# Kernel tuning notes

Hardware: AMD Instinct MI355X
Metric: run time of the kernel (lower is better)

Reference implementation:

```python
import jax, jax.numpy as jnp
import numpy as np

# PEPS hyper-parameters (match init_kwargs)
L1 = 6
L2 = 6
D_PHYS = 2   # d: physical dimension
D_BOND = 6   # D: virtual bond dimension
DC = 24      # Dc: boundary-MPS truncation cutoff
BATCH = 32


def setup_inputs() -> dict:
    key = jax.random.key(0)
    k1, k2 = jax.random.split(key)
    tensors = jax.random.normal(
        k1, (L1, L2, D_PHYS, D_BOND, D_BOND, D_BOND, D_BOND), dtype=jnp.float32)
    configs = jax.random.randint(k2, (BATCH, L1 * L2), 0, D_PHYS, dtype=jnp.int32)
    return {"configs": configs, "tensors": tensors}


def _site(tensors, configs, l1, l2):
    # Gather per-sample site tensor: [b, left, up, down, right]
    t = tensors[l1, l2][configs[:, l1 * L2 + l2].astype(jnp.int32)]
    if l2 == 0:
        t = t[:, :1]
    if l1 == 0:
        t = t[:, :, :1]
    if l1 == L1 - 1:
        t = t[:, :, :, :1]
    if l2 == L2 - 1:
        t = t[:, :, :, :, :1]
    return t


def _qr(a):
    # Reduced QR that also supports wide matrices (m < n) in a way that has
    # a JAX-differentiable definition: Q comes from the QR of the first m
    # columns (identical to Householder QR of the full matrix), and
    # R[:, m:] = Q^T A[:, m:].
    m, n = a.shape[-2], a.shape[-1]
    if m >= n:
        return jnp.linalg.qr(a)
    q, r1 = jnp.linalg.qr(a[..., :m])
    r2 = jnp.matmul(jnp.swapaxes(q, -1, -2), a[..., m:])
    return q, jnp.concatenate([r1, r2], axis=-1)


def _bmps(line1, line2):
    # Contract row of boundary MPS with next PEPS row: [b,l,L,u,d,r,R]
    double = [jnp.einsum('blumr,bLmdR->blLudrR', t1, t2)
              for t1, t2 in zip(line1, line2)]
    b = double[0].shape[0]
    s0 = double[0].shape
    double[0] = double[0].reshape(b, s0[1] * s0[2], s0[3], s0[4], s0[5], s0[6])
    # Left-to-right QR canonicalization sweep
    for j in range(L2 - 1):
        t = double[j]
        _, l, u, dn, r, R = t.shape
        q, rmat = _qr(t.reshape(b, l * u * dn, r * R))
        k = q.shape[-1]
        double[j] = q.reshape(b, l, u, dn, k)
        remain = rmat.reshape(b, k, r, R)
        double[j + 1] = jnp.einsum('bkmM,bmMudrR->bkudrR', remain, double[j + 1])
    tlast = double[-1]
    sl = tlast.shape
    double[-1] = tlast.reshape(b, sl[1], sl[2], sl[3], sl[4] * sl[5])
    # Right-to-left truncated-SVD compression sweep
    for j in range(L2 - 1, 0, -1):
        t = double[j]
        _, l, u, dn, r = t.shape
        U, S, Vh = jnp.linalg.svd(t.reshape(b, l, u * dn * r), full_matrices=False)
        if S.shape[-1] > DC:
            U = U[:, :, :DC]
            S = S[:, :DC]
            Vh = Vh[:, :DC, :]
        double[j] = Vh.reshape(b, -1, u, dn, r)
        double[j - 1] = jnp.einsum('bludm,bmr,br->bludr', double[j - 1], U, S)
    return double


def _forward(configs, tensors):
    rows = [[_site(tensors, configs, i, j) for j in range(L2)] for i in range(L1)]
    cand = rows[0]
    for i in range(1, L1):
        cand = _bmps(cand, rows[i])
    res = cand[0]
    for j in range(1, L2):
        res = res * cand[j]  # all [b,1,1,1,1] after the final row
    return res[:, 0, 0, 0, 0]


def reference(configs, tensors):
    return _forward(configs, tensors)
```

## Files before the change

### kernel.cpp

```cpp
#include <hip/hip_runtime.h>
#include <math.h>

#define NT 1024
#define NB 32

#define M_D    0
#define M_A    124416
#define M_A3   248832
#define M_Q2   373248
#define M_Q4   404352
#define M_TB   435456
#define M_Q1   456192
#define M_Q0   457488
#define M_ROW  457552
#define M_R    463168
#define M_T    483904
#define M_T3   504640
#define M_G    525392
#define M_CA   546128
#define M_CB   554840
#define M_X    563552
#define M_Z    567008
#define M_T5   570464
#define M_X5   570680
#define M_QP   570896
#define M_X1   570960
#define M_T1   571024
#define M_Y0   571888
#define M_YH   575344
#define M_W    578800
#define M_P    579376
#define M_STRIDE 582832

__device__ __align__(16) double g_m[(size_t)NB * M_STRIDE];

#define STAGE_CAP 82944
#define LO_J     82944
#define LO_NORM  88128
#define LO_S     89280
#define LO_E     89472
#define LO_E2    90624
#define LO_SEL   91776
#define LO_FLAG  91872
#define LO_LOG   91880
#define LO_SCALE 91888
#define LDS_BYTES 92160

__device__ __forceinline__ char* ldsp() {
  extern __shared__ char lds_pool[];
  return lds_pool;
}
#define L_B(p)     ((float*)(p))
#define L_J(p)     ((float*)((p)+LO_J))
#define L_ZR(p)    ((double*)(p))
#define L_J24(p)   ((double*)((p)+28800))
#define L_NORM(p)  ((double*)((p)+LO_NORM))
#define L_S(p)     ((double*)((p)+LO_S))
#define L_E(p)     ((double*)((p)+LO_E))
#define L_E2(p)    ((double*)((p)+LO_E2))
#define L_SEL(p)   ((int*)((p)+LO_SEL))
#define L_FLAG(p)  ((int*)((p)+LO_FLAG))
#define L_LOG(p)   ((double*)((p)+LO_LOG))
#define L_SCALE(p) ((double*)((p)+LO_SCALE))

__device__ void mm_nn(const double* __restrict__ A, int lda, const double* __restrict__ Bm, int ldb,
                      double* __restrict__ C, int ldc, int M, int N, int Kd, int tid) {
  if ((N & 3) == 0) {
    int nstrip = N >> 2;
    for (int u = tid; u < M * nstrip; u += NT) {
      int i = u / nstrip, j0 = (u - i * nstrip) << 2;
      const double* a = A + (size_t)i * lda;
      const double* b = Bm + j0;
      double d0 = 0, d1 = 0, d2 = 0, d3 = 0;
      for (int k = 0; k < Kd; ++k) {
        double av = a[k];
        const double* br = b + (size_t)k * ldb;
        d0 += av * br[0]; d1 += av * br[1]; d2 += av * br[2]; d3 += av * br[3];
      }
      size_t o = (size_t)i * ldc + j0;
      C[o] = d0; C[o + 1] = d1; C[o + 2] = d2; C[o + 3] = d3;
    }
  } else {
    for (int idx = tid; idx < M * N; idx += NT) {
      int i = idx / N, j = idx - i * N;
      const double* a = A + (size_t)i * lda;
      double acc = 0.0;
      for (int k = 0; k < Kd; ++k) acc += a[k] * Bm[(size_t)k * ldb + j];
      C[(size_t)i * ldc + j] = acc;
    }
  }
  __syncthreads();
}

__device__ void mm_tn(const double* __restrict__ A, int lda, const double* __restrict__ Bm, int ldb,
                      double* __restrict__ C, int ldc, int M, int N, int Kd, int tid) {
  if ((N & 3) == 0) {
    int nstrip = N >> 2;
    for (int u = tid; u < M * nstrip; u += NT) {
      int i = u / nstrip, j0 = (u - i * nstrip) << 2;
      double d0 = 0, d1 = 0, d2 = 0, d3 = 0;
      for (int k = 0; k < Kd; ++k) {
        double av = A[(size_t)k * lda + i];
        const double* br = Bm + (size_t)k * ldb + j0;
        d0 += av * br[0]; d1 += av * br[1]; d2 += av * br[2]; d3 += av * br[3];
      }
      size_t o = (size_t)i * ldc + j0;
      C[o] = d0; C[o + 1] = d1; C[o + 2] = d2; C[o + 3] = d3;
    }
  } else {
    for (int idx = tid; idx < M * N; idx += NT) {
      int i = idx / N, j = idx - i * N;
      double acc = 0.0;
      for (int k = 0; k < Kd; ++k) acc += A[(size_t)k * lda + i] * Bm[(size_t)k * ldb + j];
      C[(size_t)i * ldc + j] = acc;
    }
  }
  __syncthreads();
}

__device__ void mm_nt(const double* __restrict__ A, int lda, const double* __restrict__ Bm, int ldb,
                      double* __restrict__ C, int ldc, int M, int N, int Kd, int tid) {
  for (int idx = tid; idx < M * N; idx += NT) {
    int i = idx / N, j = idx - i * N;
    double acc = 0.0;
    for (int k = 0; k < Kd; ++k) acc += A[(size_t)i * lda + k] * Bm[(size_t)j * ldb + k];
    C[(size_t)i * ldc + j] = acc;
  }
  __syncthreads();
}

__device__ __forceinline__ void mm_panel_compute(const double* __restrict__ A, int lda,
                                                 const double* __restrict__ SB,
                                                 double* __restrict__ C, int ldc,
                                                 int M, int n0, int nb, int Kd, int tid) {
  int nstrip = nb >> 2;
  if ((M & 3) == 0) {
    int items = (M >> 2) * nstrip;
    for (int u = tid; u < items; u += NT) {
      int iq = u / nstrip;
      int i = iq << 2;
      int jl = (u - iq * nstrip) << 2;
      const double* a0 = A + (size_t)i * lda;
      const double* a1 = a0 + lda;
      const double* a2 = a1 + lda;
      const double* a3 = a2 + lda;
      double c00=0,c01=0,c02=0,c03=0, c10=0,c11=0,c12=0,c13=0;
      double c20=0,c21=0,c22=0,c23=0, c30=0,c31=0,c32=0,c33=0;
      for (int k = 0; k < Kd; ++k) {
        const double* bp = SB + k * nb + jl;
        double b0 = bp[0], b1 = bp[1], b2 = bp[2], b3 = bp[3];
        double av0 = a0[k], av1 = a1[k], av2 = a2[k], av3 = a3[k];
        c00 += av0*b0; c01 += av0*b1; c02 += av0*b2; c03 += av0*b3;
        c10 += av1*b0; c11 += av1*b1; c12 += av1*b2; c13 += av1*b3;
        c20 += av2*b0; c21 += av2*b1; c22 += av2*b2; c23 += av2*b3;
        c30 += av3*b0; c31 += av3*b1; c32 += av3*b2; c33 += av3*b3;
      }
      size_t o0 = (size_t)i * ldc + n0 + jl;
      size_t o1 = o0 + ldc, o2 = o1 + ldc, o3 = o2 + ldc;
      C[o0]=c00; C[o0+1]=c01; C[o0+2]=c02; C[o0+3]=c03;
      C[o1]=c10; C[o1+1]=c11; C[o1+2]=c12; C[o1+3]=c13;
      C[o2]=c20; C[o2+1]=c21; C[o2+2]=c22; C[o2+3]=c23;
      C[o3]=c30; C[o3+1]=c31; C[o3+2]=c32; C[o3+3]=c33;
    }
  } else {
    int items = (M >> 1) * nstrip;
    for (int u = tid; u < items; u += NT) {
      int iq = u / nstrip;
      int i = iq << 1;
      int jl = (u - iq * nstrip) << 2;
      const double* a0 = A + (size_t)i * lda;
      const double* a1 = a0 + lda;
      double c00=0,c01=0,c02=0,c03=0, c10=0,c11=0,c12=0,c13=0;
      for (int k = 0; k < Kd; ++k) {
        const double* bp = SB + k * nb + jl;
        double b0 = bp[0], b1 = bp[1], b2 = bp[2], b3 = bp[3];
        double av0 = a0[k], av1 = a1[k];
        c00 += av0*b0; c01 += av0*b1; c02 += av0*b2; c03 += av0*b3;
        c10 += av1*b0; c11 += av1*b1; c12 += av1*b2; c13 += av1*b3;
      }
      size_t o0 = (size_t)i * ldc + n0 + jl, o1 = o0 + ldc;
      C[o0]=c00; C[o0+1]=c01; C[o0+2]=c02; C[o0+3]=c03;
      C[o1]=c10; C[o1+1]=c11; C[o1+2]=c12; C[o1+3]=c13;
    }
  }
}

__device__ void mm_nn_bs(const double* __restrict__ A, int lda,
                         const double* __restrict__ Bm, int ldb,
                         double* __restrict__ C, int ldc,
                         int M, int N, int Kd, char* lp, int tid) {
  double* SB = (double*)lp;
  for (int n0 = 0; n0 < N; n0 += 64) {
    int nb = N - n0; if (nb > 64) nb = 64;
    for (int x = tid; x < Kd * nb; x += NT) {
      int k = x / nb, j = x - k * nb;
      SB[x] = Bm[(size_t)k * ldb + n0 + j];
    }
    __syncthreads();
    mm_panel_compute(A, lda, SB, C, ldc, M, n0, nb, Kd, tid);
    __syncthreads();
  }
}

__device__ void mm_nn_bsD(const double* __restrict__ A, int lda,
                          const double* __restrict__ cand, int cl, int cr,
                          const double* __restrict__ rowS, int al, int ar,
                          double* __restrict__ C, int ldc,
                          int M, int Kd, char* lp, int tid) {
  double* SB = (double*)lp;
  int mnext = cr * ar;
  int N = 6 * mnext;
  for (int n0 = 0; n0 < N; n0 += 64) {
    int nb = N - n0; if (nb > 64) nb = 64;
    for (int x = tid; x < Kd * nb; x += NT) {
      int k = x / nb, j = x - k * nb;
      int col = n0 + j;
      int l = k / al, L = k - l * al;
      int d = col / mnext, rem = col - d * mnext;
      int rr = rem / ar, R_ = rem - rr * ar;
      double acc = 0.0;
#pragma unroll
      for (int mu = 0; mu < 6; ++mu)
        acc += cand[(l * 6 + mu) * cr + rr] * rowS[((L * 6 + mu) * 6 + d) * ar + R_];
      SB[x] = acc;
    }
    __syncthreads();
    mm_panel_compute(A, lda, SB, C, ldc, M, n0, nb, Kd, tid);
    __syncthreads();
  }
}

__device__ void gram_s(const double* __restrict__ A, int lda, int n, int Kd,
                       double* __restrict__ G, char* lp, int tid) {
  double* P = (double*)lp;
  int KC = (STAGE_CAP / 8) / n; if (KC > Kd) KC = Kd;
  for (int idx = tid; idx < n * n; idx += NT) {
    int i = idx / n, j = idx - i * n;
    if (j >= i) G[idx] = 0.0;
  }
  __syncthreads();
  for (int k0 = 0; k0 < Kd; k0 += KC) {
    int kc = Kd - k0; if (kc > KC) kc = KC;
    for (int x = tid; x < kc * n; x += NT) {
      int kk = x / n, i = x - kk * n;
      P[x] = A[(size_t)(k0 + kk) * lda + i];
    }
    __syncthreads();
    for (int idx = tid; idx < n * n; idx += NT) {
      int i = idx / n, j = idx - i * n;
      if (j < i) continue;
      double s = 0.0;
      for (int kk = 0; kk < kc; ++kk) s += P[kk * n + i] * P[kk * n + j];
      G[idx] += s;
    }
    __syncthreads();
  }
}

__device__ void cholesky(double* G, int n, int tid) {
  for (int j = 0; j < n; ++j) {
    __syncthreads();
    double piv = G[(size_t)j * n + j];
    double r = sqrt(piv > 1e-300 ? piv : 1e-300);
    double inv = 1.0 / r;
    __syncthreads();
    for (int i = j + tid; i < n; i += NT)
      G[(size_t)j * n + i] = (i == j) ? r : G[(size_t)j * n + i] * inv;
    __syncthreads();
    int w = n - j - 1;
    for (int idx = tid; idx < w * w; idx += NT) {
      int ii = idx / w, kk = idx - ii * w;
      int i = j + 1 + ii, k2 = j + 1 + kk;
      if (k2 >= i) G[(size_t)i * n + k2] -= G[(size_t)j * n + i] * G[(size_t)j * n + k2];
    }
  }
  __syncthreads();
}

__device__ void trinv(const double* G, int n, double* T, int tid) {
  for (int c = tid; c < n; c += NT) {
    T[(size_t)c * n + c] = 1.0 / G[(size_t)c * n + c];
    for (int r = c - 1; r >= 0; --r) {
      double s = 0.0;
      for (int k = r + 1; k <= c; ++k) s += G[(size_t)r * n + k] * T[(size_t)k * n + c];
      T[(size_t)r * n + c] = -s / G[(size_t)r * n + r];
    }
    for (int r = c + 1; r < n; ++r) T[(size_t)r * n + c] = 0.0;
  }
  __syncthreads();
}

__device__ void copyR(const double* G, int n, double* Rw, int tid) {
  for (int idx = tid; idx < n * n; idx += NT) {
    int i = idx / n, k = idx - i * n;
    Rw[idx] = (k >= i) ? G[idx] : 0.0;
  }
  __syncthreads();
}

__device__ void tallQR(const double* A, int Mr, int Nc, double* Q, double* Rw,
                       double* G, double* T, char* lp, int tid) {
  if (Mr >= 128) gram_s(A, Nc, Nc, Mr, G, lp, tid);
  else           mm_tn(A, Nc, A, Nc, G, Nc, Nc, Nc, Mr, tid);
  cholesky(G, Nc, tid);
  trinv(G, Nc, T, tid);
  if (Q) {
    if (Nc >= 64) mm_nn_bs(A, Nc, T, Nc, Q, Nc, Mr, Nc, Nc, lp, tid);
    else          mm_nn(A, Nc, T, Nc, Q, Nc, Mr, Nc, Nc, tid);
  }
  if (Rw) copyR(G, Nc, Rw, tid);
}

__device__ void wideQR(const double* A, int Mr, int Nc, double* Q, double* Rw,
                       double* G, double* T, int tid) {
  mm_tn(A, Nc, A, Nc, G, Mr, Mr, Mr, Mr, tid);
  cholesky(G, Mr, tid);
  trinv(G, Mr, T, tid);
  mm_nn(A, Nc, T, Mr, Q, Mr, Mr, Mr, Mr, tid);
  mm_tn(Q, Mr, A, Nc, Rw, Nc, Mr, Nc, Mr, tid);
}

__device__ void build_D(const double* __restrict__ cand, int cl, int cr,
                        const double* __restrict__ rowS, int al, int ar,
                        double* __restrict__ D, int tid) {
  int mnext = cr * ar;
  int ncols = 6 * mnext;
  int n = cl * al * ncols;
  for (int idx = tid; idx < n; idx += NT) {
    int row = idx / ncols, col = idx - row * ncols;
    int l = row / al, L = row - l * al;
    int d = col / mnext, rem = col - d * mnext;
    int rr = rem / ar, R_ = rem - rr * ar;
    double acc = 0.0;
#pragma unroll
    for (int mu = 0; mu < 6; ++mu)
      acc += cand[(l * 6 + mu) * cr + rr] * rowS[((L * 6 + mu) * 6 + d) * ar + R_];
    D[idx] = acc;
  }
  __syncthreads();
}

__device__ void gather_row(const int* cfg, const float* tens, int b, int r, int dd,
                           double* ROW, const int* roff, int tid) {
  for (int j = 0; j < 6; ++j) {
    int al = (j == 0) ? 1 : 6, ar = (j == 5) ? 1 : 6;
    const float* base = tens + (size_t)(((r * 6 + j) * 2 + cfg[b * 36 + r * 6 + j])) * 1296;
    int n = al * 6 * dd * ar;
    double* dst = ROW + roff[j];
    for (int idx = tid; idx < n; idx += NT) {
      int R_ = idx % ar; int t2 = idx / ar;
      int d = t2 % dd; t2 /= dd;
      int mu = t2 % 6; int L = t2 / 6;
      dst[idx] = (double)base[L * 216 + mu * 36 + d * 6 + R_];
    }
  }
  __syncthreads();
}

__device__ void jacobi36(float* B, int R, float* J, int* flag, int tid) {
  for (int i = tid; i < 36 * 36; i += NT) J[i] = ((i / 36) == (i % 36)) ? 1.f : 0.f;
  __syncthreads();
  for (int sw = 0; sw < 9; ++sw) {
    if (tid == 0) *flag = 0;
    __syncthreads();
    for (int t = 0; t < 35; ++t) {
      int s = tid >> 4, h = tid & 15;
      bool act = (tid < 288);
      int p = 0, q = 0; float c = 1.f, sn = 0.f; bool doit = false;
      if (act) {
        if (s == 0) { p = 35; q = t % 35; }
        else { p = (t + s) % 35; q = (t - s + 35) % 35; }
        float app = 0.f, aqq = 0.f, apq = 0.f;
        for (int r = h; r < R; r += 16) {
          float x = B[r * 36 + p], y = B[r * 36 + q];
          app += x * x; aqq += y * y; apq += x * y;
        }
        app += __shfl_xor(app, 1); aqq += __shfl_xor(aqq, 1); apq += __shfl_xor(apq, 1);
        app += __shfl_xor(app, 2); aqq += __shfl_xor(aqq, 2); apq += __shfl_xor(apq, 2);
        app += __shfl_xor(app, 4); aqq += __shfl_xor(aqq, 4); apq += __shfl_xor(apq, 4);
        app += __shfl_xor(app, 8); aqq += __shfl_xor(aqq, 8); apq += __shfl_xor(apq, 8);
        double g = (double)apq, aa = (double)app, bb = (double)aqq;
        if (g * g > 1e-14 * aa * bb) {
          doit = true;
          if (h == 0) *flag = 1;
          double tau = (bb - aa) / (2.0 * g);
          double tt = (tau >= 0.0 ? 1.0 : -1.0) / (fabs(tau) + sqrt(1.0 + tau * tau));
          double cc = 1.0 / sqrt(1.0 + tt * tt);
          c = (float)cc; sn = (float)(tt * cc);
        }
      }
      if (doit) {
        for (int r = h; r < R; r += 16) {
          float x = B[r * 36 + p], y = B[r * 36 + q];
          B[r * 36 + p] = c * x - sn * y;
          B[r * 36 + q] = sn * x + c * y;
        }
        for (int r = h; r < 36; r += 16) {
          float x = J[r * 36 + p], y = J[r * 36 + q];
          J[r * 36 + p] = c * x - sn * y;
          J[r * 36 + q] = sn * x + c * y;
        }
      }
      __syncthreads();
    }
    int f = *flag;
    __syncthreads();
    if (!f) break;
  }
}

#define J144LD 145
__device__ void jacobi144(float* B, int* flag, int tid) {
  for (int sw = 0; sw < 9; ++sw) {
    if (tid == 0) *flag = 0;
    __syncthreads();
    for (int t = 0; t < 143; ++t) {
      int s = tid >> 3, h = tid & 7;
      bool act = (tid < 576);
      float xp[18], xq[18];
      int p = 0, q = 0; float c = 1.f, sn = 0.f; bool doit = false;
      if (act) {
        if (s == 0) { p = 143; q = t % 143; }
        else { p = (t + s) % 143; q = (t - s + 143) % 143; }
        float app = 0.f, aqq = 0.f, apq = 0.f;
#pragma unroll
        for (int i = 0; i < 18; ++i) {
          int r = h + 8 * i;
          float x = B[r * J144LD + p], y = B[r * J144LD + q];
          xp[i] = x; xq[i] = y;
          app += x * x; aqq += y * y; apq += x * y;
        }
        app += __shfl_xor(app, 1); aqq += __shfl_xor(aqq, 1); apq += __shfl_xor(apq, 1);
        app += __shfl_xor(app, 2); aqq += __shfl_xor(aqq, 2); apq += __shfl_xor(apq, 2);
        app += __shfl_xor(app, 4); aqq += __shfl_xor(aqq, 4); apq += __shfl_xor(apq, 4);
        double g = (double)apq, aa = (double)app, bb = (double)aqq;
        if (g * g > 1e-14 * aa * bb) {
          doit = true;
          if (h == 0) *flag = 1;
          double tau = (bb - aa) / (2.0 * g);
          double tt = (tau >= 0.0 ? 1.0 : -1.0) / (fabs(tau) + sqrt(1.0 + tau * tau));
          double cc = 1.0 / sqrt(1.0 + tt * tt);
          c = (float)cc; sn = (float)(tt * cc);
        }
      }
      if (doit) {
#pragma unroll
        for (int i = 0; i < 18; ++i) {
          int r = h + 8 * i;
          B[r * J144LD + p] = c * xp[i] - sn * xq[i];
          B[r * J144LD + q] = sn * xp[i] + c * xq[i];
        }
      }
      __syncthreads();
    }
    int f = *flag;
    __syncthreads();
    if (!f) break;
  }
}

__device__ void colnorms_sel(const float* B, int R, int C, int ldb, int keep, char* lp, int tid) {
  double* NORM = L_NORM(lp); int* SEL = L_SEL(lp); double* S = L_S(lp);
  for (int c = tid; c < C; c += NT) {
    double a = 0.0;
    for (int r = 0; r < R; ++r) { float v = B[r * ldb + c]; a += (double)v * (double)v; }
    NORM[c] = a;
  }
  __syncthreads();
  if (tid == 0) {
    for (int i = 0; i < keep; ++i) {
      int bi = 0; double bv = -1.0;
      for (int x = 0; x < C; ++x) if (NORM[x] > bv) { bv = NORM[x]; bi = x; }
      SEL[i] = bi;
      S[i] = sqrt(bv > 1e-300 ? bv : 1e-300);
      NORM[bi] = -2.0;
    }
  }
  __syncthreads();
}

#define ZLD 25
__device__ void jacobi24d(double* Z, int R, double* J24, int* flag, int tid) {
  for (int i = tid; i < 576; i += NT) J24[i] = ((i / 24) == (i % 24)) ? 1.0 : 0.0;
  __syncthreads();
  for (int sw = 0; sw < 16; ++sw) {
    if (tid == 0) *flag = 0;
    __syncthreads();
    for (int t = 0; t < 23; ++t) {
      int s = tid >> 4, h = tid & 15;
      bool act = (tid < 192);
      int p = 0, q = 0; double c_ = 1.0, sn = 0.0; bool doit = false;
      if (act) {
        if (s == 0) { p = 23; q = t % 23; }
        else { p = (t + s) % 23; q = (t - s + 23) % 23; }
        double app = 0, aqq = 0, apq = 0;
        for (int r = h; r < R; r += 16) {
          double x = Z[r * ZLD + p], y = Z[r * ZLD + q];
          app += x * x; aqq += y * y; apq += x * y;
        }
        app += __shfl_xor(app, 1); aqq += __shfl_xor(aqq, 1); apq += __shfl_xor(apq, 1);
        app += __shfl_xor(app, 2); aqq += __shfl_xor(aqq, 2); apq += __shfl_xor(apq, 2);
        app += __shfl_xor(app, 4); aqq += __shfl_xor(aqq, 4); apq += __shfl_xor(apq, 4);
        app += __shfl_xor(app, 8); aqq += __shfl_xor(aqq, 8); apq += __shfl_xor(apq, 8);
        if (apq * apq > 1e-28 * app * aqq) {
          doit = true;
          if (h == 0) *flag = 1;
          double tau = (aqq - app) / (2.0 * apq);
          double tt = (tau >= 0.0 ? 1.0 : -1.0) / (fabs(tau) + sqrt(1.0 + tau * tau));
          double cc = 1.0 / sqrt(1.0 + tt * tt);
          c_ = cc; sn = tt * cc;
        }
      }
      if (doit) {
        for (int r = h; r < R; r += 16) {
          double x = Z[r * ZLD + p], y = Z[r * ZLD + q];
          Z[r * ZLD + p] = c_ * x - sn * y;
          Z[r * ZLD + q] = sn * x + c_ * y;
        }
        for (int r = h; r < 24; r += 16) {
          double x = J24[r * 24 + p], y = J24[r * 24 + q];
          J24[r * 24 + p] = c_ * x - sn * y;
          J24[r * 24 + q] = sn * x + c_ * y;
        }
      }
      __syncthreads();
    }
    int f = *flag;
    __syncthreads();
    if (!f) break;
  }
}

__device__ void sort24(const double* Z, int R, char* lp, int tid) {
  double* NORM = L_NORM(lp); int* SEL = L_SEL(lp); double* S = L_S(lp);
  for (int c = tid; c < 24; c += NT) {
    double a = 0.0;
    for (int r = 0; r < R; ++r) { double v = Z[r * ZLD + c]; a += v * v; }
    NORM[c] = a;
  }
  __syncthreads();
  if (tid == 0) {
    for (int i = 0; i < 24; ++i) {
      int bi = 0; double bv = -1.0;
      for (int x = 0; x < 24; ++x) if (NORM[x] > bv) { bv = NORM[x]; bi = x; }
      SEL[i] = bi;
      S[i] = sqrt(bv > 1e-300 ? bv : 1e-300);
      NORM[bi] = -2.0;
    }
  }
  __syncthreads();
}

__device__ void refine(const double* t, int tR, int tC, int My, int ucase,
                       double* site, double* X, double* Dd, char* lp, int tid) {
  double* G = Dd + M_G;   double* T24 = Dd + M_T;
  double* Y0 = Dd + M_Y0; double* YH = Dd + M_YH;
  double* W = Dd + M_W;   double* P = Dd + M_P;
  double* Zr = L_ZR(lp);  double* J24 = L_J24(lp);
  int Rz = ucase ? tC : tR;
  mm_tn(Y0, 24, Y0, 24, G, 24, 24, 24, My, tid);
  cholesky(G, 24, tid);
  trinv(G, 24, T24, tid);
  mm_nn(Y0, 24, T24, 24, YH, 24, My, 24, 24, tid);
  if (ucase) mm_tn(t, tC, YH, 24, Zr, ZLD, tC, 24, tR, tid);
  else       mm_nn(t, tC, YH, 24, Zr, ZLD, tR, 24, tC, tid);
  jacobi24d(Zr, Rz, J24, L_FLAG(lp), tid);
  sort24(Zr, Rz, lp, tid);
  int* SEL = L_SEL(lp); double* S = L_S(lp);
  for (int i = tid; i < 576; i += NT) {
    int k = i / 24, c = i - k * 24;
    W[i] = J24[k * 24 + SEL[c]];
  }
  __syncthreads();
  mm_nn(YH, 24, W, 24, P, 24, My, 24, 24, tid);
  if (ucase) {
    for (int i = tid; i < My * 24; i += NT) {
      int k = i / 24, c = i - k * 24;
      X[i] = P[i] * S[c];
    }
    for (int i = tid; i < 24 * tC; i += NT) {
      int c = i / tC, x = i - c * tC;
      site[i] = Zr[x * ZLD + SEL[c]] / S[c];
    }
  } else {
    for (int i = tid; i < 24 * My; i += NT) {
      int c = i / My, x = i - c * My;
      site[i] = P[x * 24 + c];
    }
    for (int i = tid; i < Rz * 24; i += NT) {
      int k = i / 24, c = i - k * 24;
      X[i] = Zr[k * ZLD + SEL[c]];
    }
  }
  __syncthreads();
}

__device__ void svdV36d(const double* t, int R, double* site, double* X,
                        double* Dd, char* lp, int tid) {
  float* B = L_B(lp); float* J = L_J(lp);
  for (int i = tid; i < R * 36; i += NT) B[i] = (float)t[i];
  __syncthreads();
  jacobi36(B, R, J, L_FLAG(lp), tid);
  colnorms_sel(B, R, 36, 36, 24, lp, tid);
  int* SEL = L_SEL(lp);
  double* Y0 = Dd + M_Y0;
  for (int i = tid; i < 36 * 24; i += NT) {
    int x = i / 24, c = i - x * 24;
    Y0[i] = (double)J[x * 36 + SEL[c]];
  }
  __syncthreads();
  refine(t, R, 36, 36, 0, site, X, Dd, lp, tid);
}

__device__ void svdU36d(const double* t, double* site, double* X,
                        double* Dd, char* lp, int tid) {
  float* B = L_B(lp); float* J = L_J(lp);
  for (int i = tid; i < 144 * 36; i += NT) {
    int x = i / 36, k = i - x * 36;
    B[i] = (float)t[k * 144 + x];
  }
  __syncthreads();
  jacobi36(B, 144, J, L_FLAG(lp), tid);
  colnorms_sel(B, 144, 36, 36, 24, lp, tid);
  int* SEL = L_SEL(lp);
  double* Y0 = Dd + M_Y0;
  for (int i = tid; i < 36 * 24; i += NT) {
    int x = i / 24, c = i - x * 24;
    Y0[i] = (double)J[x * 36 + SEL[c]];
  }
  __syncthreads();
  refine(t, 36, 144, 36, 1, site, X, Dd, lp, tid);
}

__device__ void stepJ3bigd(const double* t, double* site, double* X,
                           double* Dd, char* lp, int tid) {
  float* B = L_B(lp);
  for (int i = tid; i < 144 * 144; i += NT) {
    int r = i / 144, c = i - r * 144;
    B[r * J144LD + c] = (float)t[i];
  }
  __syncthreads();
  jacobi144(B, L_FLAG(lp), tid);
  colnorms_sel(B, 144, 144, J144LD, 24, lp, tid);
  int* SEL = L_SEL(lp);
  double* Y0 = Dd + M_Y0;
  for (int i = tid; i < 144 * 24; i += NT) {
    int k = i / 24, c = i - k * 24;
    Y0[i] = (double)B[k * J144LD + SEL[c]];
  }
  __syncthreads();
  refine(t, 144, 144, 144, 1, site, X, Dd, lp, tid);
}

__device__ void stepJ5(const double* t5, double* G, double* T, double* Qp,
                       double* cand5, double* X5, int tid) {
  mm_nt(t5, 6, t5, 6, G, 6, 6, 6, 6, tid);
  cholesky(G, 6, tid);
  trinv(G, 6, T, tid);
  mm_tn(t5, 6, T, 6, Qp, 6, 6, 6, 6, tid);
  for (int i = tid; i < 36; i += NT) {
    int l = i / 6, mu = i - l * 6;
    cand5[i] = Qp[mu * 6 + l];
  }
  __syncthreads();
  mm_nn(t5, 6, Qp, 6, X5, 6, 36, 6, 6, tid);
}

__device__ void stepJ1(const double* t1, double* G, double* T,
                       double* cand1, double* X1, int tid) {
  mm_nt(t1, 144, t1, 144, G, 6, 6, 6, 144, tid);
  cholesky(G, 6, tid);
  trinv(G, 6, T, tid);
  mm_tn(T, 6, t1, 144, cand1, 144, 6, 144, 6, tid);
  for (int i = tid; i < 36; i += NT) {
    int r = i / 6, c = i - r * 6;
    X1[i] = (c <= r) ? G[c * 6 + r] : 0.0;
  }
  __syncthreads();
}

__device__ void rescale0(double* cout_, char* lp, int tid) {
  if (tid == 0) {
    double m = 0.0;
    for (int i = 0; i < 36; ++i) { double v = fabs(cout_[i]); if (v > m) m = v; }
    if (!(m > 1e-300)) m = 1.0;
    *L_SCALE(lp) = m;
    *L_LOG(lp) += log(m);
  }
  __syncthreads();
  double m = *L_SCALE(lp);
  for (int i = tid; i < 36; i += NT) cout_[i] /= m;
  __syncthreads();
}

__device__ void run_round(int r, int b, const int* cfg, const float* tens,
                          const double* cin_, double* cout_, int tid) {
  char* lp = ldsp();
  double* Dd = g_m + (size_t)b * M_STRIDE;
  const int K  = (r == 1) ? 36 : 144;
  const int cK = (r == 1) ? 6 : 24;
  int cb[7] = {1, 6, cK, cK, cK, 6, 1};
  int co[6]; co[0] = 0;
  for (int j = 0; j < 5; ++j) co[j + 1] = co[j] + cb[j] * 6 * cb[j + 1];
  const int ob[7] = {1, 6, 24, 24, 24, 6, 1};
  int oo[6]; oo[0] = 0;
  for (int j = 0; j < 5; ++j) oo[j + 1] = oo[j] + ob[j] * 6 * ob[j + 1];
  const int roff6[6] = {0, 216, 1512, 2808, 4104, 5400};

  double* ROW = Dd + M_ROW;
  double* Dbuf = Dd + M_D;  double* Abuf = Dd + M_A;  double* A3 = Dd + M_A3;
  double* Q2 = Dd + M_Q2;   double* Q4 = Dd + M_Q4;   double* Q1 = Dd + M_Q1;  double* Q0 = Dd + M_Q0;
  double* TB = Dd + M_TB;   double* Rw = Dd + M_R;    double* Tw = Dd + M_T;   double* T3 = Dd + M_T3;
  double* G = Dd + M_G;     double* X = Dd + M_X;     double* Zp = Dd + M_Z;
  double* t5 = Dd + M_T5;   double* X5 = Dd + M_X5;   double* Qp = Dd + M_QP;
  double* X1 = Dd + M_X1;   double* t1 = Dd + M_T1;

  gather_row(cfg, tens, b, r, 6, ROW, roff6, tid);

  build_D(cin_ + co[0], 1, cb[1], ROW + roff6[0], 1, 6, Dbuf, tid);
  wideQR(Dbuf, 6, 36, Q0, Rw, G, Tw, tid);

  mm_nn_bsD(Rw, 36, cin_ + co[1], 6, cb[2], ROW + roff6[1], 6, 6,
            Abuf, 6 * K, 6, 36, lp, tid);
  if (K == 36) tallQR(Abuf, 36, 36, Q1, Rw, G, Tw, lp, tid);
  else         wideQR(Abuf, 36, 144, Q1, Rw, G, Tw, tid);

  mm_nn_bsD(Rw, K, cin_ + co[2], cb[2], cb[3], ROW + roff6[2], 6, 6,
            Abuf, 6 * K, 36, K, lp, tid);
  tallQR(Abuf, 216, K, Q2, Rw, G, Tw, lp, tid);

  mm_nn_bsD(Rw, K, cin_ + co[3], cb[3], cb[4], ROW + roff6[3], 6, 6,
            A3, 6 * K, K, K, lp, tid);
  tallQR(A3, 6 * K, K, nullptr, Rw, G, T3, lp, tid);

  mm_nn_bsD(Rw, K, cin_ + co[4], cb[4], cb[5], ROW + roff6[4], 6, 6,
            Abuf, 216, K, K, lp, tid);
  tallQR(Abuf, 6 * K, 36, Q4, Rw, G, Tw, lp, tid);

  build_D(cin_ + co[5], cb[5], 1, ROW + roff6[5], 6, 1, Dbuf, tid);
  mm_nn(Rw, 36, Dbuf, 6, t5, 6, 36, 6, 36, tid);

  stepJ5(t5, G, Tw, Qp, cout_ + oo[5], X5, tid);
  mm_nn(Q4, 36, X5, 6, TB, 6, 6 * K, 6, 36, tid);
  svdV36d(TB, K, cout_ + oo[4], X, Dd, lp, tid);
  mm_nn_bs(T3, K, X, 24, Zp, 24, K, 24, K, lp, tid);
  mm_nn_bs(A3, K, Zp, 24, TB, 24, 6 * K, 24, K, lp, tid);
  if (K == 144) stepJ3bigd(TB, cout_ + oo[3], X, Dd, lp, tid);
  else          svdU36d(TB, cout_ + oo[3], X, Dd, lp, tid);
  mm_nn_bs(Q2, K, X, 24, TB, 24, 216, 24, K, lp, tid);
  svdU36d(TB, cout_ + oo[2], X, Dd, lp, tid);
  mm_nn(Q1, 36, X, 24, t1, 24, 36, 24, 36, tid);
  stepJ1(t1, G, Tw, cout_ + oo[1], X1, tid);
  mm_nn(Q0, 6, X1, 6, cout_ + oo[0], 6, 6, 6, 6, tid);
  rescale0(cout_, lp, tid);
}

extern "C" __global__ void __launch_bounds__(NT, 4)
peps_kernel(const int* __restrict__ cfg, const float* __restrict__ tens, float* __restrict__ out) {
  const int b = blockIdx.x;
  const int tid = threadIdx.x;
  char* lp = ldsp();
  double* CA = g_m + (size_t)b * M_STRIDE + M_CA;
  double* CB = g_m + (size_t)b * M_STRIDE + M_CB;
  if (tid == 0) *L_LOG(lp) = 0.0;

  {
    const int c1off[6] = {0, 36, 252, 468, 684, 900};
    for (int j = 0; j < 6; ++j) {
      int al = (j == 0) ? 1 : 6, ar = (j == 5) ? 1 : 6;
      const float* base = tens + (size_t)((j * 2 + cfg[b * 36 + j])) * 1296;
      int n = al * 6 * ar;
      double* dst = CA + c1off[j];
      for (int idx = tid; idx < n; idx += NT) {
        int l = idx / (6 * ar); int rest = idx - l * (6 * ar);
        int mu = rest / ar; int rr = rest - mu * ar;
        dst[idx] = (double)base[l * 216 + mu * 6 + rr];
      }
    }
    __syncthreads();
  }

  run_round(1, b, cfg, tens, CA, CB, tid);
  run_round(2, b, cfg, tens, CB, CA, tid);
  run_round(3, b, cfg, tens, CA, CB, tid);
  run_round(4, b, cfg, tens, CB, CA, tid);

  {
    const int roff1[6] = {0, 36, 252, 468, 684, 900};
    double* ROW = g_m + (size_t)b * M_STRIDE + M_ROW;
    gather_row(cfg, tens, b, 5, 1, ROW, roff1, tid);
    double* E = L_E(lp); double* E2 = L_E2(lp);
    if (tid == 0) E[0] = 1.0;
    __syncthreads();
    const int ob[7] = {1, 6, 24, 24, 24, 6, 1};
    int oo[6]; oo[0] = 0;
    for (int j = 0; j < 5; ++j) oo[j + 1] = oo[j] + ob[j] * 6 * ob[j + 1];
    const double* candF = CA;
    double* src = E; double* dst = E2;
    for (int j = 0; j < 6; ++j) {
      int cl = ob[j], cr = ob[j + 1];
      int al = (j == 0) ? 1 : 6, ar = (j == 5) ? 1 : 6;
      int n = cr * ar;
      for (int idx = tid; idx < n; idx += NT) {
        int rr = idx / ar, R_ = idx - rr * ar;
        double acc = 0.0;
        for (int l = 0; l < cl; ++l) {
          for (int L = 0; L < al; ++L) {
            double e = src[l * al + L];
            double s2 = 0.0;
#pragma unroll
            for (int mu = 0; mu < 6; ++mu)
              s2 += candF[oo[j] + (l * 6 + mu) * cr + rr] * ROW[roff1[j] + (L * 6 + mu) * ar + R_];
            acc += e * s2;
          }
        }
        dst[idx] = acc;
      }
      __syncthreads();
      double* tmp = src; src = dst; dst = tmp;
    }
    if (tid == 0) out[b] = (float)(src[0] * exp(*L_LOG(lp)));
  }
}

extern "C" void kernel_launch(void* const* d_in, const int* in_sizes, int n_in,
                              void* d_out, int out_size, void* d_ws, size_t ws_size,
                              hipStream_t stream) {
  (void)in_sizes; (void)n_in; (void)out_size; (void)d_ws; (void)ws_size;
  const int* cfg = (const int*)d_in[0];
  const float* tens = (const float*)d_in[1];
  float* out = (float*)d_out;
  (void)hipFuncSetAttribute((const void*)peps_kernel,
                            hipFuncAttributeMaxDynamicSharedMemorySize, LDS_BYTES);
  peps_kernel<<<dim3(NB), dim3(NT), LDS_BYTES, stream>>>(cfg, tens, out);
}
```

Measured before the change: 34.56 ms.

## Split monolithic per-sample kernel into multi-kernel pipeline with multi-block matmuls

Replaces the single 32-block kernel (one block per sample running all rounds) with a sequence of smaller kernels per round. The heavy matmul, Gram and Q-multiply stages now spread each sample over several blocks (panels or strided work), so more CUs are used than the 32 the old launch occupied. The serial steps (Cholesky, SVD) stay one block per sample. This adds many kernel launches per call and round-trips through global memory between stages, and the log accumulator moves to a global array.

Result: faster. 30.19 ms (-12.6%).

```diff
diff --git a/kernel.cpp b/kernel.cpp
--- a/kernel.cpp
+++ b/kernel.cpp
@@ -33,18 +33,14 @@
 #define M_STRIDE 582832
 
 __device__ __align__(16) double g_m[(size_t)NB * M_STRIDE];
-
-#define STAGE_CAP 82944
+__device__ double g_log[NB];
+
 #define LO_J     82944
 #define LO_NORM  88128
 #define LO_S     89280
-#define LO_E     89472
-#define LO_E2    90624
-#define LO_SEL   91776
-#define LO_FLAG  91872
-#define LO_LOG   91880
-#define LO_SCALE 91888
-#define LDS_BYTES 92160
+#define LO_SEL   89472
+#define LO_FLAG  89568
+#define SVD_LDS  92160
 
 __device__ __forceinline__ char* ldsp() {
   extern __shared__ char lds_pool[];
@@ -56,12 +52,8 @@
 #define L_J24(p)   ((double*)((p)+28800))
 #define L_NORM(p)  ((double*)((p)+LO_NORM))
 #define L_S(p)     ((double*)((p)+LO_S))
-#define L_E(p)     ((double*)((p)+LO_E))
-#define L_E2(p)    ((double*)((p)+LO_E2))
 #define L_SEL(p)   ((int*)((p)+LO_SEL))
 #define L_FLAG(p)  ((int*)((p)+LO_FLAG))
-#define L_LOG(p)   ((double*)((p)+LO_LOG))
-#define L_SCALE(p) ((double*)((p)+LO_SCALE))
 
 __device__ void mm_nn(const double* __restrict__ A, int lda, const double* __restrict__ Bm, int ldb,
                       double* __restrict__ C, int ldc, int M, int N, int Kd, int tid) {
@@ -185,23 +177,6 @@
   }
 }
 
-__device__ void mm_nn_bs(const double* __restrict__ A, int lda,
-                         const double* __restrict__ Bm, int ldb,
-                         double* __restrict__ C, int ldc,
-                         int M, int N, int Kd, char* lp, int tid) {
-  double* SB = (double*)lp;
-  for (int n0 = 0; n0 < N; n0 += 64) {
-    int nb = N - n0; if (nb > 64) nb = 64;
-    for (int x = tid; x < Kd * nb; x += NT) {
-      int k = x / nb, j = x - k * nb;
-      SB[x] = Bm[(size_t)k * ldb + n0 + j];
-    }
-    __syncthreads();
-    mm_panel_compute(A, lda, SB, C, ldc, M, n0, nb, Kd, tid);
-    __syncthreads();
-  }
-}
-
 __device__ void mm_nn_bsD(const double* __restrict__ A, int lda,
                           const double* __restrict__ cand, int cl, int cr,
                           const double* __restrict__ rowS, int al, int ar,
@@ -230,33 +205,6 @@
   }
 }
 
-__device__ void gram_s(const double* __restrict__ A, int lda, int n, int Kd,
-                       double* __restrict__ G, char* lp, int tid) {
-  double* P = (double*)lp;
-  int KC = (STAGE_CAP / 8) / n; if (KC > Kd) KC = Kd;
-  for (int idx = tid; idx < n * n; idx += NT) {
-    int i = idx / n, j = idx - i * n;
-    if (j >= i) G[idx] = 0.0;
-  }
-  __syncthreads();
-  for (int k0 = 0; k0 < Kd; k0 += KC) {
-    int kc = Kd - k0; if (kc > KC) kc = KC;
-    for (int x = tid; x < kc * n; x += NT) {
-      int kk = x / n, i = x - kk * n;
-      P[x] = A[(size_t)(k0 + kk) * lda + i];
-    }
-    __syncthreads();
-    for (int idx = tid; idx < n * n; idx += NT) {
-      int i = idx / n, j = idx - i * n;
-      if (j < i) continue;
-      double s = 0.0;
-      for (int kk = 0; kk < kc; ++kk) s += P[kk * n + i] * P[kk * n + j];
-      G[idx] += s;
-    }
-    __syncthreads();
-  }
-}
-
 __device__ void cholesky(double* G, int n, int tid) {
   for (int j = 0; j < n; ++j) {
     __syncthreads();
@@ -298,17 +246,13 @@
   __syncthreads();
 }
 
-__device__ void tallQR(const double* A, int Mr, int Nc, double* Q, double* Rw,
-                       double* G, double* T, char* lp, int tid) {
-  if (Mr >= 128) gram_s(A, Nc, Nc, Mr, G, lp, tid);
-  else           mm_tn(A, Nc, A, Nc, G, Nc, Nc, Nc, Mr, tid);
+__device__ void tallQR_small(const double* A, int Mr, int Nc, double* Q, double* Rw,
+                             double* G, double* T, int tid) {
+  mm_tn(A, Nc, A, Nc, G, Nc, Nc, Nc, Mr, tid);
   cholesky(G, Nc, tid);
   trinv(G, Nc, T, tid);
-  if (Q) {
-    if (Nc >= 64) mm_nn_bs(A, Nc, T, Nc, Q, Nc, Mr, Nc, Nc, lp, tid);
-    else          mm_nn(A, Nc, T, Nc, Q, Nc, Mr, Nc, Nc, tid);
-  }
-  if (Rw) copyR(G, Nc, Rw, tid);
+  mm_nn(A, Nc, T, Nc, Q, Nc, Mr, Nc, Nc, tid);
+  copyR(G, Nc, Rw, tid);
 }
 
 __device__ void wideQR(const double* A, int Mr, int Nc, double* Q, double* Rw,
@@ -679,148 +623,250 @@
   __syncthreads();
 }
 
-__device__ void rescale0(double* cout_, char* lp, int tid) {
+
+extern "C" __global__ void __launch_bounds__(NT)
+k_init(const int* __restrict__ cfg, const float* __restrict__ tens) {
+  int b = blockIdx.x, tid = threadIdx.x;
+  double* CA = g_m + (size_t)b * M_STRIDE + M_CA;
+  if (tid == 0) g_log[b] = 0.0;
+  const int c1off[6] = {0, 36, 252, 468, 684, 900};
+  for (int j = 0; j < 6; ++j) {
+    int al = (j == 0) ? 1 : 6, ar = (j == 5) ? 1 : 6;
+    const float* base = tens + (size_t)((j * 2 + cfg[b * 36 + j])) * 1296;
+    int n = al * 6 * ar;
+    double* dst = CA + c1off[j];
+    for (int idx = tid; idx < n; idx += NT) {
+      int l = idx / (6 * ar); int rest = idx - l * (6 * ar);
+      int mu = rest / ar; int rr = rest - mu * ar;
+      dst[idx] = (double)base[l * 216 + mu * 6 + rr];
+    }
+  }
+}
+
+extern "C" __global__ void __launch_bounds__(NT)
+k_pre(const int* __restrict__ cfg, const float* __restrict__ tens,
+      int r, int K, int cin_off, int co1) {
+  int b = blockIdx.x, tid = threadIdx.x;
+  char* lp = ldsp();
+  double* Dd = g_m + (size_t)b * M_STRIDE;
+  const double* cin_ = Dd + cin_off;
+  const int roff6[6] = {0, 216, 1512, 2808, 4104, 5400};
+  int cK = (K == 36) ? 6 : 24;
+  double* ROW = Dd + M_ROW; double* Dbuf = Dd + M_D; double* Abuf = Dd + M_A;
+  double* Q0 = Dd + M_Q0; double* Q1 = Dd + M_Q1;
+  double* Rw = Dd + M_R;  double* Tw = Dd + M_T; double* G = Dd + M_G;
+  gather_row(cfg, tens, b, r, 6, ROW, roff6, tid);
+  build_D(cin_, 1, 6, ROW, 1, 6, Dbuf, tid);
+  wideQR(Dbuf, 6, 36, Q0, Rw, G, Tw, tid);
+  mm_nn_bsD(Rw, 36, cin_ + co1, 6, cK, ROW + 216, 6, 6, Abuf, 6 * K, 6, 36, lp, tid);
+  if (K == 36) tallQR_small(Abuf, 36, 36, Q1, Rw, G, Tw, tid);
+  else         wideQR(Abuf, 36, 144, Q1, Rw, G, Tw, tid);
+}
+
+extern "C" __global__ void __launch_bounds__(NT)
+k_bsD(int NP, int cin_off, int coj, int cl, int cr, int rowoff,
+      int dst_off, int ldc, int M, int Kd) {
+  int b = blockIdx.x / NP, p = blockIdx.x % NP;
+  int tid = threadIdx.x;
+  double* Dd = g_m + (size_t)b * M_STRIDE;
+  const double* cand = Dd + cin_off + coj;
+  const double* rowS = Dd + M_ROW + rowoff;
+  const double* A = Dd + M_R;
+  double* C = Dd + dst_off;
+  double* SB = (double*)ldsp();
+  int mnext = cr * 6;
+  int N = 6 * mnext;
+  int n0 = p * 64;
+  int nb = N - n0; if (nb > 64) nb = 64;
+  for (int x = tid; x < Kd * nb; x += NT) {
+    int k = x / nb, j = x - k * nb;
+    int col = n0 + j;
+    int l = k / 6, L = k - l * 6;
+    int d = col / mnext, rem = col - d * mnext;
+    int rr = rem / 6, R_ = rem - rr * 6;
+    double acc = 0.0;
+#pragma unroll
+    for (int mu = 0; mu < 6; ++mu)
+      acc += cand[(l * 6 + mu) * cr + rr] * rowS[((L * 6 + mu) * 6 + d) * 6 + R_];
+    SB[x] = acc;
+  }
+  __syncthreads();
+  mm_panel_compute(A, Kd, SB, C, ldc, M, n0, nb, Kd, tid);
+}
+
+extern "C" __global__ void __launch_bounds__(NT)
+k_gram(int NG, int src_off, int nc, int Mr) {
+  int b = blockIdx.x / NG, w = blockIdx.x % NG;
+  int gt = w * NT + threadIdx.x, gs = NG * NT;
+  const double* A = g_m + (size_t)b * M_STRIDE + src_off;
+  double* G = g_m + (size_t)b * M_STRIDE + M_G;
+  int nstrip = nc >> 2;
+  for (int u = gt; u < nc * nstrip; u += gs) {
+    int i = u / nstrip, j0 = (u - i * nstrip) << 2;
+    if (j0 + 3 < i) continue;
+    double d0 = 0, d1 = 0, d2 = 0, d3 = 0;
+    for (int k = 0; k < Mr; ++k) {
+      double a = A[(size_t)k * nc + i];
+      const double* br = A + (size_t)k * nc + j0;
+      d0 += a * br[0]; d1 += a * br[1]; d2 += a * br[2]; d3 += a * br[3];
+    }
+    if (j0 >= i)     G[(size_t)i * nc + j0]     = d0;
+    if (j0 + 1 >= i) G[(size_t)i * nc + j0 + 1] = d1;
+    if (j0 + 2 >= i) G[(size_t)i * nc + j0 + 2] = d2;
+    G[(size_t)i * nc + j0 + 3] = d3;
+  }
+}
+
+extern "C" __global__ void __launch_bounds__(NT)
+k_choltrinv(int n, int T_off) {
+  int b = blockIdx.x, tid = threadIdx.x;
+  double* G = g_m + (size_t)b * M_STRIDE + M_G;
+  double* T = g_m + (size_t)b * M_STRIDE + T_off;
+  double* Rw = g_m + (size_t)b * M_STRIDE + M_R;
+  cholesky(G, n, tid);
+  trinv(G, n, T, tid);
+  copyR(G, n, Rw, tid);
+}
+
+extern "C" __global__ void __launch_bounds__(NT)
+k_qmultp(int NP, int A_off, int T_off, int Q_off, int M, int n) {
+  int b = blockIdx.x / NP, p = blockIdx.x % NP;
+  int tid = threadIdx.x;
+  double* Dd = g_m + (size_t)b * M_STRIDE;
+  const double* A = Dd + A_off;
+  const double* T = Dd + T_off;
+  double* Q = Dd + Q_off;
+  double* SB = (double*)ldsp();
+  int n0 = p * 64, nb = n - n0; if (nb > 64) nb = 64;
+  for (int x = tid; x < n * nb; x += NT) {
+    int k = x / nb, j = x - k * nb;
+    SB[x] = T[(size_t)k * n + n0 + j];
+  }
+  __syncthreads();
+  mm_panel_compute(A, n, SB, Q, n, M, n0, nb, n, tid);
+}
+
+extern "C" __global__ void __launch_bounds__(NT)
+k_mmflat(int NW, int A_off, int lda, int B_off, int ldb, int C_off, int ldc,
+         int M, int N, int Kd) {
+  int b = blockIdx.x / NW, w = blockIdx.x % NW;
+  int gt = w * NT + threadIdx.x, gs = NW * NT;
+  double* Dd = g_m + (size_t)b * M_STRIDE;
+  const double* A = Dd + A_off;
+  const double* Bm = Dd + B_off;
+  double* C = Dd + C_off;
+  if ((N & 3) == 0) {
+    int nstrip = N >> 2;
+    for (int u = gt; u < M * nstrip; u += gs) {
+      int i = u / nstrip, j0 = (u - i * nstrip) << 2;
+      const double* a = A + (size_t)i * lda;
+      const double* bp = Bm + j0;
+      double d0 = 0, d1 = 0, d2 = 0, d3 = 0;
+      for (int k = 0; k < Kd; ++k) {
+        double av = a[k];
+        const double* br = bp + (size_t)k * ldb;
+        d0 += av * br[0]; d1 += av * br[1]; d2 += av * br[2]; d3 += av * br[3];
+      }
+      size_t o = (size_t)i * ldc + j0;
+      C[o] = d0; C[o + 1] = d1; C[o + 2] = d2; C[o + 3] = d3;
+    }
+  } else {
+    for (int idx = gt; idx < M * N; idx += gs) {
+      int i = idx / N, j = idx - i * N;
+      const double* a = A + (size_t)i * lda;
+      double acc = 0.0;
+      for (int k = 0; k < Kd; ++k) acc += a[k] * Bm[(size_t)k * ldb + j];
+      C[(size_t)i * ldc + j] = acc;
+    }
+  }
+}
+
+extern "C" __global__ void __launch_bounds__(NT)
+k_j5(int cin_off, int co5, int cout_off) {
+  int b = blockIdx.x, tid = threadIdx.x;
+  double* Dd = g_m + (size_t)b * M_STRIDE;
+  build_D(Dd + cin_off + co5, 6, 1, Dd + M_ROW + 5400, 6, 1, Dd + M_D, tid);
+  mm_nn(Dd + M_R, 36, Dd + M_D, 6, Dd + M_T5, 6, 36, 6, 36, tid);
+  stepJ5(Dd + M_T5, Dd + M_G, Dd + M_T, Dd + M_QP, Dd + cout_off + 8676, Dd + M_X5, tid);
+}
+
+extern "C" __global__ void __launch_bounds__(NT)
+k_svd(int mode, int K, int site_off, int X_off) {
+  int b = blockIdx.x, tid = threadIdx.x;
+  char* lp = ldsp();
+  double* Dd = g_m + (size_t)b * M_STRIDE;
+  const double* t = Dd + M_TB;
+  double* site = Dd + site_off;
+  double* X = Dd + X_off;
+  if (mode == 0) {
+    svdV36d(t, K, site, X, Dd, lp, tid);
+  } else if (mode == 1) {
+    if (K == 144) stepJ3bigd(t, site, X, Dd, lp, tid);
+    else          svdU36d(t, site, X, Dd, lp, tid);
+  } else {
+    svdU36d(t, site, X, Dd, lp, tid);
+  }
+}
+
+extern "C" __global__ void __launch_bounds__(NT)
+k_tail(int cout_off) {
+  int b = blockIdx.x, tid = threadIdx.x;
+  double* Dd = g_m + (size_t)b * M_STRIDE;
+  mm_nn(Dd + M_Q1, 36, Dd + M_X, 24, Dd + M_T1, 24, 36, 24, 36, tid);
+  stepJ1(Dd + M_T1, Dd + M_G, Dd + M_T, Dd + cout_off + 36, Dd + M_X1, tid);
+  mm_nn(Dd + M_Q0, 6, Dd + M_X1, 6, Dd + cout_off, 6, 6, 6, 6, tid);
+  __shared__ double sc;
+  double* cout_ = Dd + cout_off;
   if (tid == 0) {
     double m = 0.0;
     for (int i = 0; i < 36; ++i) { double v = fabs(cout_[i]); if (v > m) m = v; }
     if (!(m > 1e-300)) m = 1.0;
-    *L_SCALE(lp) = m;
-    *L_LOG(lp) += log(m);
-  }
-  __syncthreads();
-  double m = *L_SCALE(lp);
+    sc = m;
+    g_log[b] += log(m);
+  }
+  __syncthreads();
+  double m = sc;
   for (int i = tid; i < 36; i += NT) cout_[i] /= m;
-  __syncthreads();
-}
-
-__device__ void run_round(int r, int b, const int* cfg, const float* tens,
-                          const double* cin_, double* cout_, int tid) {
-  char* lp = ldsp();
+}
+
+extern "C" __global__ void __launch_bounds__(NT)
+k_final(const int* __restrict__ cfg, const float* __restrict__ tens, float* __restrict__ out) {
+  int b = blockIdx.x, tid = threadIdx.x;
+  __shared__ double E[144], E2[144];
   double* Dd = g_m + (size_t)b * M_STRIDE;
-  const int K  = (r == 1) ? 36 : 144;
-  const int cK = (r == 1) ? 6 : 24;
-  int cb[7] = {1, 6, cK, cK, cK, 6, 1};
-  int co[6]; co[0] = 0;
-  for (int j = 0; j < 5; ++j) co[j + 1] = co[j] + cb[j] * 6 * cb[j + 1];
+  const int roff1[6] = {0, 36, 252, 468, 684, 900};
+  double* ROW = Dd + M_ROW;
+  gather_row(cfg, tens, b, 5, 1, ROW, roff1, tid);
+  if (tid == 0) E[0] = 1.0;
+  __syncthreads();
   const int ob[7] = {1, 6, 24, 24, 24, 6, 1};
   int oo[6]; oo[0] = 0;
   for (int j = 0; j < 5; ++j) oo[j + 1] = oo[j] + ob[j] * 6 * ob[j + 1];
-  const int roff6[6] = {0, 216, 1512, 2808, 4104, 5400};
-
-  double* ROW = Dd + M_ROW;
-  double* Dbuf = Dd + M_D;  double* Abuf = Dd + M_A;  double* A3 = Dd + M_A3;
-  double* Q2 = Dd + M_Q2;   double* Q4 = Dd + M_Q4;   double* Q1 = Dd + M_Q1;  double* Q0 = Dd + M_Q0;
-  double* TB = Dd + M_TB;   double* Rw = Dd + M_R;    double* Tw = Dd + M_T;   double* T3 = Dd + M_T3;
-  double* G = Dd + M_G;     double* X = Dd + M_X;     double* Zp = Dd + M_Z;
-  double* t5 = Dd + M_T5;   double* X5 = Dd + M_X5;   double* Qp = Dd + M_QP;
-  double* X1 = Dd + M_X1;   double* t1 = Dd + M_T1;
-
-  gather_row(cfg, tens, b, r, 6, ROW, roff6, tid);
-
-  build_D(cin_ + co[0], 1, cb[1], ROW + roff6[0], 1, 6, Dbuf, tid);
-  wideQR(Dbuf, 6, 36, Q0, Rw, G, Tw, tid);
-
-  mm_nn_bsD(Rw, 36, cin_ + co[1], 6, cb[2], ROW + roff6[1], 6, 6,
-            Abuf, 6 * K, 6, 36, lp, tid);
-  if (K == 36) tallQR(Abuf, 36, 36, Q1, Rw, G, Tw, lp, tid);
-  else         wideQR(Abuf, 36, 144, Q1, Rw, G, Tw, tid);
-
-  mm_nn_bsD(Rw, K, cin_ + co[2], cb[2], cb[3], ROW + roff6[2], 6, 6,
-            Abuf, 6 * K, 36, K, lp, tid);
-  tallQR(Abuf, 216, K, Q2, Rw, G, Tw, lp, tid);
-
-  mm_nn_bsD(Rw, K, cin_ + co[3], cb[3], cb[4], ROW + roff6[3], 6, 6,
-            A3, 6 * K, K, K, lp, tid);
-  tallQR(A3, 6 * K, K, nullptr, Rw, G, T3, lp, tid);
-
-  mm_nn_bsD(Rw, K, cin_ + co[4], cb[4], cb[5], ROW + roff6[4], 6, 6,
-            Abuf, 216, K, K, lp, tid);
-  tallQR(Abuf, 6 * K, 36, Q4, Rw, G, Tw, lp, tid);
-
-  build_D(cin_ + co[5], cb[5], 1, ROW + roff6[5], 6, 1, Dbuf, tid);
-  mm_nn(Rw, 36, Dbuf, 6, t5, 6, 36, 6, 36, tid);
-
-  stepJ5(t5, G, Tw, Qp, cout_ + oo[5], X5, tid);
-  mm_nn(Q4, 36, X5, 6, TB, 6, 6 * K, 6, 36, tid);
-  svdV36d(TB, K, cout_ + oo[4], X, Dd, lp, tid);
-  mm_nn_bs(T3, K, X, 24, Zp, 24, K, 24, K, lp, tid);
-  mm_nn_bs(A3, K, Zp, 24, TB, 24, 6 * K, 24, K, lp, tid);
-  if (K == 144) stepJ3bigd(TB, cout_ + oo[3], X, Dd, lp, tid);
-  else          svdU36d(TB, cout_ + oo[3], X, Dd, lp, tid);
-  mm_nn_bs(Q2, K, X, 24, TB, 24, 216, 24, K, lp, tid);
-  svdU36d(TB, cout_ + oo[2], X, Dd, lp, tid);
-  mm_nn(Q1, 36, X, 24, t1, 24, 36, 24, 36, tid);
-  stepJ1(t1, G, Tw, cout_ + oo[1], X1, tid);
-  mm_nn(Q0, 6, X1, 6, cout_ + oo[0], 6, 6, 6, 6, tid);
-  rescale0(cout_, lp, tid);
-}
-
-extern "C" __global__ void __launch_bounds__(NT, 4)
-peps_kernel(const int* __restrict__ cfg, const float* __restrict__ tens, float* __restrict__ out) {
-  const int b = blockIdx.x;
-  const int tid = threadIdx.x;
-  char* lp = ldsp();
-  double* CA = g_m + (size_t)b * M_STRIDE + M_CA;
-  double* CB = g_m + (size_t)b * M_STRIDE + M_CB;
-  if (tid == 0) *L_LOG(lp) = 0.0;
-
-  {
-    const int c1off[6] = {0, 36, 252, 468, 684, 900};
-    for (int j = 0; j < 6; ++j) {
-      int al = (j == 0) ? 1 : 6, ar = (j == 5) ? 1 : 6;
-      const float* base = tens + (size_t)((j * 2 + cfg[b * 36 + j])) * 1296;
-      int n = al * 6 * ar;
-      double* dst = CA + c1off[j];
-      for (int idx = tid; idx < n; idx += NT) {
-        int l = idx / (6 * ar); int rest = idx - l * (6 * ar);
-        int mu = rest / ar; int rr = rest - mu * ar;
-        dst[idx] = (double)base[l * 216 + mu * 6 + rr];
-      }
-    }
-    __syncthreads();
-  }
-
-  run_round(1, b, cfg, tens, CA, CB, tid);
-  run_round(2, b, cfg, tens, CB, CA, tid);
-  run_round(3, b, cfg, tens, CA, CB, tid);
-  run_round(4, b, cfg, tens, CB, CA, tid);
-
-  {
-    const int roff1[6] = {0, 36, 252, 468, 684, 900};
-    double* ROW = g_m + (size_t)b * M_STRIDE + M_ROW;
-    gather_row(cfg, tens, b, 5, 1, ROW, roff1, tid);
-    double* E = L_E(lp); double* E2 = L_E2(lp);
-    if (tid == 0) E[0] = 1.0;
-    __syncthreads();
-    const int ob[7] = {1, 6, 24, 24, 24, 6, 1};
-    int oo[6]; oo[0] = 0;
-    for (int j = 0; j < 5; ++j) oo[j + 1] = oo[j] + ob[j] * 6 * ob[j + 1];
-    const double* candF = CA;
-    double* src = E; double* dst = E2;
-    for (int j = 0; j < 6; ++j) {
-      int cl = ob[j], cr = ob[j + 1];
-      int al = (j == 0) ? 1 : 6, ar = (j == 5) ? 1 : 6;
-      int n = cr * ar;
-      for (int idx = tid; idx < n; idx += NT) {
-        int rr = idx / ar, R_ = idx - rr * ar;
-        double acc = 0.0;
-        for (int l = 0; l < cl; ++l) {
-          for (int L = 0; L < al; ++L) {
-            double e = src[l * al + L];
-            double s2 = 0.0;
+  const double* candF = Dd + M_CA;
+  double* src = E; double* dst = E2;
+  for (int j = 0; j < 6; ++j) {
+    int cl = ob[j], cr = ob[j + 1];
+    int al = (j == 0) ? 1 : 6, ar = (j == 5) ? 1 : 6;
+    int n = cr * ar;
+    for (int idx = tid; idx < n; idx += NT) {
+      int rr = idx / ar, R_ = idx - rr * ar;
+      double acc = 0.0;
+      for (int l = 0; l < cl; ++l) {
+        for (int L = 0; L < al; ++L) {
+          double e = src[l * al + L];
+          double s2 = 0.0;
 #pragma unroll
-            for (int mu = 0; mu < 6; ++mu)
-              s2 += candF[oo[j] + (l * 6 + mu) * cr + rr] * ROW[roff1[j] + (L * 6 + mu) * ar + R_];
-            acc += e * s2;
-          }
-        }
-        dst[idx] = acc;
-      }
-      __syncthreads();
-      double* tmp = src; src = dst; dst = tmp;
-    }
-    if (tid == 0) out[b] = (float)(src[0] * exp(*L_LOG(lp)));
-  }
+          for (int mu = 0; mu < 6; ++mu)
+            s2 += candF[oo[j] + (l * 6 + mu) * cr + rr] * ROW[roff1[j] + (L * 6 + mu) * ar + R_];
+          acc += e * s2;
+        }
+      }
+      dst[idx] = acc;
+    }
+    __syncthreads();
+    double* tmp = src; src = dst; dst = tmp;
+  }
+  if (tid == 0) out[b] = (float)(src[0] * exp(g_log[b]));
 }
 
 extern "C" void kernel_launch(void* const* d_in, const int* in_sizes, int n_in,
@@ -830,7 +876,62 @@
   const int* cfg = (const int*)d_in[0];
   const float* tens = (const float*)d_in[1];
   float* out = (float*)d_out;
-  (void)hipFuncSetAttribute((const void*)peps_kernel,
-                            hipFuncAttributeMaxDynamicSharedMemorySize, LDS_BYTES);
-  peps_kernel<<<dim3(NB), dim3(NT), LDS_BYTES, stream>>>(cfg, tens, out);
-}
+
+  (void)hipFuncSetAttribute((const void*)k_svd,
+                            hipFuncAttributeMaxDynamicSharedMemorySize, SVD_LDS);
+  (void)hipFuncSetAttribute((const void*)k_bsD,
+                            hipFuncAttributeMaxDynamicSharedMemorySize, 73728);
+  (void)hipFuncSetAttribute((const void*)k_qmultp,
+                            hipFuncAttributeMaxDynamicSharedMemorySize, 73728);
+
+  hipLaunchKernelGGL(k_init, dim3(NB), dim3(NT), 0, stream, cfg, tens);
+
+  for (int r = 1; r <= 4; ++r) {
+    int K = (r == 1) ? 36 : 144;
+    int cK = (r == 1) ? 6 : 24;
+    int cin = (r & 1) ? M_CA : M_CB;
+    int cout = (r & 1) ? M_CB : M_CA;
+    int co1 = 36;
+    int co2 = co1 + 36 * cK;
+    int co3 = co2 + cK * 6 * cK;
+    int co4 = co3 + cK * 6 * cK;
+    int co5 = co4 + cK * 36;
+    int NP = (36 * cK + 63) / 64;
+
+    hipLaunchKernelGGL(k_pre, dim3(NB), dim3(NT), 18432, stream, cfg, tens, r, K, cin, co1);
+    hipLaunchKernelGGL(k_bsD, dim3(NB * NP), dim3(NT), 73728, stream,
+                       NP, cin, co2, cK, cK, 1512, M_A, 6 * K, 36, K);
+    hipLaunchKernelGGL(k_gram, dim3(NB * 8), dim3(NT), 0, stream, 8, M_A, K, 216);
+    hipLaunchKernelGGL(k_choltrinv, dim3(NB), dim3(NT), 0, stream, K, M_T);
+    if (K == 144)
+      hipLaunchKernelGGL(k_qmultp, dim3(NB * 3), dim3(NT), 73728, stream,
+                         3, M_A, M_T, M_Q2, 216, 144);
+    else
+      hipLaunchKernelGGL(k_mmflat, dim3(NB * 4), dim3(NT), 0, stream,
+                         4, M_A, 36, M_T, 36, M_Q2, 36, 216, 36, 36);
+    hipLaunchKernelGGL(k_bsD, dim3(NB * NP), dim3(NT), 73728, stream,
+                       NP, cin, co3, cK, cK, 2808, M_A3, 6 * K, K, K);
+    hipLaunchKernelGGL(k_gram, dim3(NB * 8), dim3(NT), 0, stream, 8, M_A3, K, 6 * K);
+    hipLaunchKernelGGL(k_choltrinv, dim3(NB), dim3(NT), 0, stream, K, M_T3);
+    hipLaunchKernelGGL(k_bsD, dim3(NB * 4), dim3(NT), 73728, stream,
+                       4, cin, co4, cK, 6, 4104, M_A, 216, K, K);
+    hipLaunchKernelGGL(k_gram, dim3(NB * 8), dim3(NT), 0, stream, 8, M_A, 36, 6 * K);
+    hipLaunchKernelGGL(k_choltrinv, dim3(NB), dim3(NT), 0, stream, 36, M_T);
+    hipLaunchKernelGGL(k_mmflat, dim3(NB * 8), dim3(NT), 0, stream,
+                       8, M_A, 36, M_T, 36, M_Q4, 36, 6 * K, 36, 36);
+    hipLaunchKernelGGL(k_j5, dim3(NB), dim3(NT), 0, stream, cin, co5, cout);
+    hipLaunchKernelGGL(k_mmflat, dim3(NB * 8), dim3(NT), 0, stream,
+                       8, M_Q4, 36, M_X5, 6, M_TB, 6, 6 * K, 6, 36);
+    hipLaunchKernelGGL(k_svd, dim3(NB), dim3(NT), SVD_LDS, stream, 0, K, cout + 7812, M_X);
+    hipLaunchKernelGGL(k_mmflat, dim3(NB * 8), dim3(NT), 0, stream,
+                       8, M_T3, K, M_X, 24, M_Z, 24, K, 24, K);
+    hipLaunchKernelGGL(k_mmflat, dim3(NB * 8), dim3(NT), 0, stream,
+                       8, M_A3, K, M_Z, 24, M_TB, 24, 6 * K, 24, K);
+    hipLaunchKernelGGL(k_svd, dim3(NB), dim3(NT), SVD_LDS, stream, 1, K, cout + 4356, M_X);
+    hipLaunchKernelGGL(k_mmflat, dim3(NB * 8), dim3(NT), 0, stream,
+                       8, M_Q2, K, M_X, 24, M_TB, 24, 216, 24, K);
+    hipLaunchKernelGGL(k_svd, dim3(NB), dim3(NT), SVD_LDS, stream, 2, K, cout + 900, M_X);
+    hipLaunchKernelGGL(k_tail, dim3(NB), dim3(NT), 0, stream, cout);
+  }
+  hipLaunchKernelGGL(k_final, dim3(NB), dim3(NT), 0, stream, cfg, tens, out);
+}
```
